# Performance work log

Hardware: AMD Instinct MI355X
Metric: run time of the kernel (lower is better)

Reference implementation:

```python
import jax, jax.numpy as jnp
import numpy as np

N_NODES = 100000
N_EDGES = 1250000
FEAT = 64
HID = 10
MOD = 10.0


def setup_inputs() -> dict:
    key = jax.random.key(0)
    ks = jax.random.split(key, 12)
    inp = {
        "X": jax.random.normal(ks[0], (N_NODES, FEAT), dtype=jnp.float32),
        "W2_0": jax.random.normal(ks[1], (2 * FEAT, HID), dtype=jnp.float32) * 0.1,
        "W1_0": jax.random.normal(ks[2], (HID, HID), dtype=jnp.float32) * 0.3,
        "W2_1": jax.random.normal(ks[3], (2 * HID, HID), dtype=jnp.float32) * 0.3,
        "W1_1": jax.random.normal(ks[4], (HID, HID), dtype=jnp.float32) * 0.3,
        "W2_2": jax.random.normal(ks[5], (2 * HID, HID), dtype=jnp.float32) * 0.3,
        "W1_2": jax.random.normal(ks[6], (HID, HID), dtype=jnp.float32) * 0.3,
        "Wf1": jax.random.normal(ks[7], (HID, FEAT), dtype=jnp.float32) * 0.3,
        "Wf2": jax.random.normal(ks[8], (FEAT, FEAT), dtype=jnp.float32) * 0.1,
        "edge_src": jax.random.randint(ks[9], (N_EDGES,), 0, N_NODES, dtype=jnp.int64 if jax.config.jax_enable_x64 else jnp.int32),
        "edge_dst": jax.random.randint(ks[10], (N_EDGES,), 0, N_NODES, dtype=jnp.int64 if jax.config.jax_enable_x64 else jnp.int32),
    }
    return inp


def _rgcn_layer(X, W2, W1, src, dst):
    # gather target (i) and source (j) node features per edge: [E, in_dim]
    X_i = X[dst]
    X_j = X[src]
    # message: dense_2(relu) then dense_1(relu), divided by mod
    m = jax.nn.relu(jnp.concatenate([X_i, X_j], axis=-1) @ W2)
    m = jax.nn.relu(m @ W1) / MOD  # [E, HID]
    # sum-aggregate messages at target nodes
    agg = jax.ops.segment_sum(m, dst, num_segments=N_NODES)
    # layer activation='relu' (identity here since messages are nonneg, kept for fidelity)
    return jax.nn.relu(agg)


def reference(X, W2_0, W1_0, W2_1, W1_1, W2_2, W1_2, Wf1, Wf2, edge_src, edge_dst):
    h = X
    for W2, W1 in ((W2_0, W1_0), (W2_1, W1_1), (W2_2, W1_2)):
        h = _rgcn_layer(h, W2, W1, edge_src, edge_dst)
    h = jax.nn.relu(h @ Wf1)
    h = jax.nn.relu(h @ Wf2)
    return h
```

## Files before the change

### kernel.cpp

```cpp
#include <hip/hip_runtime.h>
#include <hip/hip_bf16.h>
#include <hip/hip_fp16.h>

#define FEAT 64
#define HID 10
#define RS 16
#define BRS 4
#define EPB 1024
#define BSH 6
#define CHK 32

typedef __attribute__((ext_vector_type(2))) float f32x2;

#if defined(__has_builtin)
#if __has_builtin(__builtin_elementwise_fma)
#define HAVE_EW_FMA 1
#endif
#endif

__device__ __forceinline__ f32x2 pk_fma(f32x2 a, f32x2 b, f32x2 c) {
#ifdef HAVE_EW_FMA
    return __builtin_elementwise_fma(a, b, c);
#else
    f32x2 r; r.x = fmaf(a.x, b.x, c.x); r.y = fmaf(a.y, b.y, c.y); return r;
#endif
}
__device__ __forceinline__ f32x2 pk_max0(f32x2 a) {
    f32x2 r; r.x = fmaxf(a.x, 0.f); r.y = fmaxf(a.y, 0.f); return r;
}

__device__ __forceinline__ unsigned int f2fp12(float v) {
    unsigned short h = __half_as_ushort(__float2half(v));
    return (((unsigned int)h) + 8u) >> 4;
}
__device__ __forceinline__ float fp12f(unsigned int f) {
    return __half2float(__ushort_as_half((unsigned short)(f << 4)));
}
__device__ __forceinline__ uint4 pack10(const float* b) {
    unsigned int f[10];
#pragma unroll
    for (int i = 0; i < 10; i++) f[i] = f2fp12(b[i]);
    uint4 d;
    d.x = f[0] | (f[1] << 12) | (f[2] << 24);
    d.y = (f[2] >> 8) | (f[3] << 4) | (f[4] << 16) | (f[5] << 28);
    d.z = (f[5] >> 4) | (f[6] << 8) | (f[7] << 20);
    d.w = f[8] | (f[9] << 12);
    return d;
}

__global__ __launch_bounds__(256) void pre_l0(
    const float* __restrict__ X,
    const float* __restrict__ W2,
    float* __restrict__ A,
    unsigned int* __restrict__ Bt,
    int n_nodes)
{
    __shared__ float w2[128 * 10];
    for (int i = threadIdx.x; i < 1280; i += 256) w2[i] = W2[i];
    __syncthreads();

    int n = blockIdx.x * 256 + threadIdx.x;
    if (n >= n_nodes) return;

    const float4* xr = reinterpret_cast<const float4*>(X + (size_t)n * FEAT);
    float a[10], b[10];
#pragma unroll
    for (int h = 0; h < 10; h++) { a[h] = 0.f; b[h] = 0.f; }

#pragma unroll
    for (int blk = 0; blk < 16; blk++) {
        float4 u = xr[blk];
        float xv[4] = { u.x, u.y, u.z, u.w };
#pragma unroll
        for (int j = 0; j < 4; j++) {
            int k = blk * 4 + j;
#pragma unroll
            for (int h = 0; h < 10; h++) {
                a[h] = fmaf(xv[j], w2[k * 10 + h], a[h]);
                b[h] = fmaf(xv[j], w2[(64 + k) * 10 + h], b[h]);
            }
        }
    }

    float4* Ar = reinterpret_cast<float4*>(A + (size_t)n * RS);
    Ar[0] = make_float4(a[0], a[1], a[2], a[3]);
    Ar[1] = make_float4(a[4], a[5], a[6], a[7]);
    Ar[2] = make_float4(a[8], a[9], 0.f, 0.f);
    *reinterpret_cast<uint4*>(Bt + (size_t)n * BRS) = pack10(b);
}


__global__ __launch_bounds__(256) void bin_hist_k(
    const int* __restrict__ dst, int* __restrict__ blockhist, int n_edges, int nbk)
{
    extern __shared__ int hist[];
    for (int i = threadIdx.x; i < nbk; i += 256) hist[i] = 0;
    __syncthreads();
    int base = blockIdx.x * EPB;
    for (int i = threadIdx.x; i < EPB; i += 256) {
        int e = base + i;
        if (e < n_edges) atomicAdd(&hist[dst[e] >> BSH], 1);
    }
    __syncthreads();
    int* row = blockhist + (size_t)blockIdx.x * nbk;
    for (int i = threadIdx.x; i < nbk; i += 256) row[i] = hist[i];
}

__global__ __launch_bounds__(256) void colchunk_sum_k(
    const int* __restrict__ blockhist, int* __restrict__ chunksum,
    int nbk, int nblk, int nchk)
{
    int b = blockIdx.x * 256 + threadIdx.x;
    int c = blockIdx.y;
    if (b >= nbk) return;
    int k0 = c * CHK;
    int k1 = min(k0 + CHK, nblk);
    int s = 0;
    for (int k = k0; k < k1; k++) s += blockhist[(size_t)k * nbk + b];
    chunksum[(size_t)b * nchk + c] = s;
}

__global__ __launch_bounds__(256) void chunk_scan_k(
    int* __restrict__ chunksum, int* __restrict__ btot, int nbk, int nchk)
{
    int b = blockIdx.x * 256 + threadIdx.x;
    if (b >= nbk) return;
    int run = 0;
    int* row = chunksum + (size_t)b * nchk;
    for (int c = 0; c < nchk; c++) {
        int v = row[c];
        row[c] = run;
        run += v;
    }
    btot[b] = run;
}

__global__ __launch_bounds__(256) void scan_k(
    const int* __restrict__ btot, int* __restrict__ bbase,
    int* __restrict__ bucket_start, int* __restrict__ start,
    int nbk, int n_nodes, int n_edges)
{
    __shared__ int ts[256];
    int t = threadIdx.x;
    int v[8];
    int s = 0;
#pragma unroll
    for (int j = 0; j < 8; j++) {
        int idx = t * 8 + j;
        v[j] = (idx < nbk) ? btot[idx] : 0;
        s += v[j];
    }
    ts[t] = s;
    __syncthreads();
    for (int off = 1; off < 256; off <<= 1) {
        int x = (t >= off) ? ts[t - off] : 0;
        __syncthreads();
        ts[t] += x;
        __syncthreads();
    }
    int run = ts[t] - s;
#pragma unroll
    for (int j = 0; j < 8; j++) {
        int idx = t * 8 + j;
        if (idx < nbk) { bbase[idx] = run; bucket_start[idx] = run; }
        run += v[j];
    }
    if (t == 255) { bucket_start[nbk] = n_edges; start[n_nodes] = n_edges; }
}

__global__ __launch_bounds__(256) void col_off2_k(
    int* __restrict__ blockhist, const int* __restrict__ chunksum,
    const int* __restrict__ bbase, int nbk, int nblk, int nchk)
{
    int b = blockIdx.x * 256 + threadIdx.x;
    int c = blockIdx.y;
    if (b >= nbk) return;
    int k0 = c * CHK;
    int k1 = min(k0 + CHK, nblk);
    int run = bbase[b] + chunksum[(size_t)b * nchk + c];
    for (int k = k0; k < k1; k++) {
        size_t idx = (size_t)k * nbk + b;
        int v = blockhist[idx];
        blockhist[idx] = run;
        run += v;
    }
}

__global__ __launch_bounds__(256) void bin_scatter_k(
    const int* __restrict__ src, const int* __restrict__ dst,
    const int* __restrict__ blockhist, int* __restrict__ packed,
    int n_edges, int nbk)
{
    extern __shared__ int cur[];
    const int* row = blockhist + (size_t)blockIdx.x * nbk;
    for (int i = threadIdx.x; i < nbk; i += 256) cur[i] = row[i];
    __syncthreads();
    int base = blockIdx.x * EPB;
    for (int i = threadIdx.x; i < EPB; i += 256) {
        int e = base + i;
        if (e < n_edges) {
            int d = dst[e];
            int pos = atomicAdd(&cur[d >> BSH], 1);
            packed[pos] = ((d & 63) << 17) | src[e];
        }
    }
}

__global__ __launch_bounds__(256) void csr_k(
    const int* __restrict__ packed, const int* __restrict__ bucket_start,
    int* __restrict__ nbr, int* __restrict__ start, int n_nodes)
{
    __shared__ int hist[64];
    __shared__ int excl[64];
    __shared__ int cur[64];
    int b = blockIdx.x;
    int base = bucket_start[b];
    int end  = bucket_start[b + 1];
    if (threadIdx.x < 64) hist[threadIdx.x] = 0;
    __syncthreads();
    for (int i = base + threadIdx.x; i < end; i += 256)
        atomicAdd(&hist[packed[i] >> 17], 1);
    __syncthreads();
    if (threadIdx.x == 0) {
        int r = 0;
        for (int k = 0; k < 64; k++) { excl[k] = r; r += hist[k]; }
    }
    __syncthreads();
    if (threadIdx.x < 64) {
        cur[threadIdx.x] = excl[threadIdx.x];
        int node = (b << 6) + threadIdx.x;
        if (node < n_nodes) start[node] = base + excl[threadIdx.x];
    }
    __syncthreads();
    for (int i = base + threadIdx.x; i < end; i += 256) {
        int p = packed[i];
        int pos = base + atomicAdd(&cur[p >> 17], 1);
        nbr[pos] = p & 0x1FFFF;
    }
}

template<bool LAST>
__global__ __launch_bounds__(256) void gather_k(
    const float* __restrict__ A,
    const unsigned int* __restrict__ Bt,
    const float* __restrict__ W1,
    const float* __restrict__ W2n,
    const int* __restrict__ start,
    const int* __restrict__ nbr,
    float* __restrict__ An,
    unsigned int* __restrict__ Bn,
    float* __restrict__ Hout,
    int n_nodes)
{
    __shared__ float w2s[200];
    if (!LAST) {
        for (int i = threadIdx.x; i < 200; i += 256) w2s[i] = W2n[i];
        __syncthreads();
    }

    f32x2 w1p[10][5];
#pragma unroll
    for (int j = 0; j < 10; j++)
#pragma unroll
        for (int h2 = 0; h2 < 5; h2++)
            w1p[j][h2] = (f32x2){ W1[j * 10 + 2 * h2], W1[j * 10 + 2 * h2 + 1] };

    int t = blockIdx.x * 256 + threadIdx.x;
    int n = t >> 2;
    int q = t & 3;
    if (n >= n_nodes) return;

    const float4* ar = reinterpret_cast<const float4*>(A + (size_t)n * RS);
    float4 a0 = ar[0], a1 = ar[1], a2 = ar[2];
    f32x2 av2[5] = { {a0.x,a0.y}, {a0.z,a0.w}, {a1.x,a1.y}, {a1.z,a1.w}, {a2.x,a2.y} };

    f32x2 acc2[5];
#pragma unroll
    for (int h2 = 0; h2 < 5; h2++) acc2[h2] = (f32x2){0.f, 0.f};

    int beg = start[n];
    int end = start[n + 1];
    for (int i = beg + q; i < end; i += 4) {
        int s = nbr[i];
        uint4 d = *reinterpret_cast<const uint4*>(Bt + (size_t)s * BRS);
        unsigned int f0 = d.x & 0xFFFu;
        unsigned int f1 = (d.x >> 12) & 0xFFFu;
        unsigned int f2 = (d.x >> 24) | ((d.y & 0xFu) << 8);
        unsigned int f3 = (d.y >> 4) & 0xFFFu;
        unsigned int f4 = (d.y >> 16) & 0xFFFu;
        unsigned int f5 = ((d.y >> 28) & 0xFu) | ((d.z & 0xFFu) << 4);
        unsigned int f6 = (d.z >> 8) & 0xFFFu;
        unsigned int f7 = d.z >> 20;
        unsigned int f8 = d.w & 0xFFFu;
        unsigned int f9 = (d.w >> 12) & 0xFFFu;

        f32x2 pre[5];
        pre[0] = av2[0] + (f32x2){ fp12f(f0), fp12f(f1) };
        pre[1] = av2[1] + (f32x2){ fp12f(f2), fp12f(f3) };
        pre[2] = av2[2] + (f32x2){ fp12f(f4), fp12f(f5) };
        pre[3] = av2[3] + (f32x2){ fp12f(f6), fp12f(f7) };
        pre[4] = av2[4] + (f32x2){ fp12f(f8), fp12f(f9) };
#pragma unroll
        for (int k = 0; k < 5; k++) pre[k] = pk_max0(pre[k]);

        f32x2 z[5];
#pragma unroll
        for (int h2 = 0; h2 < 5; h2++) z[h2] = (f32x2){0.f, 0.f};
#pragma unroll
        for (int j2 = 0; j2 < 5; j2++) {
            f32x2 pa = (f32x2){ pre[j2].x, pre[j2].x };
            f32x2 pb = (f32x2){ pre[j2].y, pre[j2].y };
#pragma unroll
            for (int h2 = 0; h2 < 5; h2++) {
                z[h2] = pk_fma(pa, w1p[2 * j2][h2], z[h2]);
                z[h2] = pk_fma(pb, w1p[2 * j2 + 1][h2], z[h2]);
            }
        }
#pragma unroll
        for (int h2 = 0; h2 < 5; h2++) acc2[h2] += pk_max0(z[h2]);
    }

#pragma unroll
    for (int h2 = 0; h2 < 5; h2++) {
        acc2[h2].x += __shfl_xor(acc2[h2].x, 1);
        acc2[h2].y += __shfl_xor(acc2[h2].y, 1);
    }
#pragma unroll
    for (int h2 = 0; h2 < 5; h2++) {
        acc2[h2].x += __shfl_xor(acc2[h2].x, 2);
        acc2[h2].y += __shfl_xor(acc2[h2].y, 2);
    }

    float hv[10];
#pragma unroll
    for (int h2 = 0; h2 < 5; h2++) {
        hv[2 * h2]     = acc2[h2].x * 0.1f;
        hv[2 * h2 + 1] = acc2[h2].y * 0.1f;
    }

    if (LAST) {
        float* Hr = Hout + (size_t)n * RS;
        if (q == 0)      *reinterpret_cast<float4*>(Hr)     = make_float4(hv[0], hv[1], hv[2], hv[3]);
        else if (q == 1) *reinterpret_cast<float4*>(Hr + 4) = make_float4(hv[4], hv[5], hv[6], hv[7]);
        else if (q == 2) *reinterpret_cast<float2*>(Hr + 8) = make_float2(hv[8], hv[9]);
    } else {
        if (q == 0) {
            float a[8];
#pragma unroll
            for (int h = 0; h < 8; h++) {
                float zz = 0.f;
#pragma unroll
                for (int k = 0; k < 10; k++) zz = fmaf(hv[k], w2s[k * 10 + h], zz);
                a[h] = zz;
            }
            float4* Ar = reinterpret_cast<float4*>(An + (size_t)n * RS);
            Ar[0] = make_float4(a[0], a[1], a[2], a[3]);
            Ar[1] = make_float4(a[4], a[5], a[6], a[7]);
        } else if (q == 1) {
            float a8 = 0.f, a9 = 0.f;
#pragma unroll
            for (int k = 0; k < 10; k++) {
                a8 = fmaf(hv[k], w2s[k * 10 + 8], a8);
                a9 = fmaf(hv[k], w2s[k * 10 + 9], a9);
            }
            *reinterpret_cast<float2*>(An + (size_t)n * RS + 8) = make_float2(a8, a9);
        } else if (q == 2) {
            float b[10];
#pragma unroll
            for (int h = 0; h < 10; h++) {
                float zz = 0.f;
#pragma unroll
                for (int k = 0; k < 10; k++) zz = fmaf(hv[k], w2s[100 + k * 10 + h], zz);
                b[h] = zz;
            }
            *reinterpret_cast<uint4*>(Bn + (size_t)n * BRS) = pack10(b);
        }
    }
}

__global__ __launch_bounds__(256) void final_k(
    const float* __restrict__ H,
    const float* __restrict__ Wf1,
    const float* __restrict__ Wf2,
    float* __restrict__ out,
    int n_nodes)
{
    __shared__ float wf1[640];
    __shared__ float wf2s[64 * 64];
    __shared__ float tT[64 * 64];

    for (int i = threadIdx.x; i < 640; i += 256) wf1[i] = Wf1[i];
    {
        const float4* w2v = reinterpret_cast<const float4*>(Wf2);
        float4* w2s = reinterpret_cast<float4*>(wf2s);
        for (int i = threadIdx.x; i < 1024; i += 256) w2s[i] = w2v[i];
    }

    int node0 = blockIdx.x * 64;

    {
        int r = threadIdx.x & 63;
        int g = threadIdx.x >> 6;
        int node = node0 + r;
        float hv[10];
        if (node < n_nodes) {
            const float4* hr = reinterpret_cast<const float4*>(H + (size_t)node * RS);
            float4 h0 = hr[0], h1 = hr[1];
            float2 h2 = *reinterpret_cast<const float2*>(H + (size_t)node * RS + 8);
            hv[0]=h0.x; hv[1]=h0.y; hv[2]=h0.z; hv[3]=h0.w;
            hv[4]=h1.x; hv[5]=h1.y; hv[6]=h1.z; hv[7]=h1.w;
            hv[8]=h2.x; hv[9]=h2.y;
        } else {
#pragma unroll
            for (int k = 0; k < 10; k++) hv[k] = 0.f;
        }
        __syncthreads();
#pragma unroll
        for (int j = 0; j < 16; j++) {
            int c = g * 16 + j;
            float v = 0.f;
#pragma unroll
            for (int k = 0; k < 10; k++) v = fmaf(hv[k], wf1[k * 64 + c], v);
            tT[c * 64 + r] = fmaxf(v, 0.f);
        }
    }
    __syncthreads();

    int r0 = (threadIdx.x >> 4) * 4;
    int c0 = (threadIdx.x & 15) * 4;
    float acc[4][4];
#pragma unroll
    for (int i = 0; i < 4; i++)
#pragma unroll
        for (int j = 0; j < 4; j++) acc[i][j] = 0.f;

    for (int k = 0; k < 64; k++) {
        float4 a = *reinterpret_cast<const float4*>(&tT[k * 64 + r0]);
        float4 b = *reinterpret_cast<const float4*>(&wf2s[k * 64 + c0]);
        float av[4] = { a.x, a.y, a.z, a.w };
        float bv[4] = { b.x, b.y, b.z, b.w };
#pragma unroll
        for (int i = 0; i < 4; i++)
#pragma unroll
            for (int j = 0; j < 4; j++)
                acc[i][j] = fmaf(av[i], bv[j], acc[i][j]);
    }

#pragma unroll
    for (int i = 0; i < 4; i++) {
        int node = node0 + r0 + i;
        if (node < n_nodes) {
            float4 o = make_float4(fmaxf(acc[i][0], 0.f), fmaxf(acc[i][1], 0.f),
                                   fmaxf(acc[i][2], 0.f), fmaxf(acc[i][3], 0.f));
            *reinterpret_cast<float4*>(&out[(size_t)node * FEAT + c0]) = o;
        }
    }
}

extern "C" void kernel_launch(void* const* d_in, const int* in_sizes, int n_in,
                              void* d_out, int out_size, void* d_ws, size_t ws_size,
                              hipStream_t stream) {
    const float* X    = (const float*)d_in[0];
    const float* W2_0 = (const float*)d_in[1];
    const float* W1_0 = (const float*)d_in[2];
    const float* W2_1 = (const float*)d_in[3];
    const float* W1_1 = (const float*)d_in[4];
    const float* W2_2 = (const float*)d_in[5];
    const float* W1_2 = (const float*)d_in[6];
    const float* Wf1  = (const float*)d_in[7];
    const float* Wf2  = (const float*)d_in[8];
    const int* src = (const int*)d_in[9];
    const int* dst = (const int*)d_in[10];
    float* out = (float*)d_out;

    const int n_edges = in_sizes[9];
    const int n_nodes = in_sizes[0] / FEAT;

    const int nbk  = (n_nodes + 63) >> 6;
    const int nblk = (n_edges + EPB - 1) / EPB;
    const int nchk = (nblk + CHK - 1) / CHK;

    const size_t h_elems = (size_t)n_nodes * RS;
    const size_t b_elems = (size_t)n_nodes * BRS;
    const size_t offH   = 0;
    const size_t offA0  = offH  + h_elems;
    const size_t offA1  = offA0 + h_elems;
    const size_t offB0  = offA1 + h_elems;
    const size_t offB1  = offB0 + b_elems;
    const size_t offNbr = offB1 + b_elems;
    const size_t offPk  = offNbr + (size_t)n_edges;
    const size_t offBh  = offPk + (size_t)n_edges;
    const size_t offCs  = offBh + (size_t)nblk * nbk;
    const size_t offBt  = offCs + (size_t)nbk * nchk;
    const size_t offBb  = offBt + (size_t)nbk;
    const size_t offBs  = offBb + (size_t)nbk;
    const size_t offSt  = offBs + (size_t)nbk + 1;

    float* H            = (float*)d_ws + offH;
    float* A0           = (float*)d_ws + offA0;
    float* A1           = (float*)d_ws + offA1;
    unsigned int* B0    = (unsigned int*)d_ws + offB0;
    unsigned int* B1    = (unsigned int*)d_ws + offB1;
    int* nbr            = (int*)d_ws + offNbr;
    int* packed         = (int*)d_ws + offPk;
    int* blockhist      = (int*)d_ws + offBh;
    int* chunksum       = (int*)d_ws + offCs;
    int* btot           = (int*)d_ws + offBt;
    int* bbase          = (int*)d_ws + offBb;
    int* bstart         = (int*)d_ws + offBs;
    int* start          = (int*)d_ws + offSt;

    const int nb = (n_nodes + 255) / 256;
    const int gb = (n_nodes * 4 + 255) / 256;
    const int fb = (n_nodes + 63) / 64;
    const int cb = (nbk + 255) / 256;
    const size_t lds_bins = (size_t)nbk * 4;

    bin_hist_k<<<nblk, 256, lds_bins, stream>>>(dst, blockhist, n_edges, nbk);
    colchunk_sum_k<<<dim3(cb, nchk), 256, 0, stream>>>(blockhist, chunksum, nbk, nblk, nchk);
    chunk_scan_k<<<cb, 256, 0, stream>>>(chunksum, btot, nbk, nchk);
    scan_k<<<1, 256, 0, stream>>>(btot, bbase, bstart, start, nbk, n_nodes, n_edges);
    col_off2_k<<<dim3(cb, nchk), 256, 0, stream>>>(blockhist, chunksum, bbase, nbk, nblk, nchk);
    bin_scatter_k<<<nblk, 256, lds_bins, stream>>>(src, dst, blockhist, packed, n_edges, nbk);
    csr_k<<<nbk, 256, 0, stream>>>(packed, bstart, nbr, start, n_nodes);

    pre_l0<<<nb, 256, 0, stream>>>(X, W2_0, A0, B0, n_nodes);
    gather_k<false><<<gb, 256, 0, stream>>>(A0, B0, W1_0, W2_1, start, nbr,
                                            A1, B1, nullptr, n_nodes);
    gather_k<false><<<gb, 256, 0, stream>>>(A1, B1, W1_1, W2_2, start, nbr,
                                            A0, B0, nullptr, n_nodes);
    gather_k<true><<<gb, 256, 0, stream>>>(A0, B0, W1_2, nullptr, start, nbr,
                                           nullptr, nullptr, H, n_nodes);

    final_k<<<fb, 256, 0, stream>>>(H, Wf1, Wf2, out, n_nodes);
}
```

Measured before the change: 249.3 us.

## Simplify CSR build with global atomics and fuse final MLP into last gather

Replaces the seven-kernel, per-block histogram counting sort with a memset, a global-atomic bucket histogram, a single scan and a global-atomic scatter. This cuts launches and the large blockhist traffic, at the cost of heavy contention on global atomics for about 1600 buckets. The last gather layer is also fused with the final two dense layers, so the H intermediate buffer and one kernel launch go away. In exchange, the fused kernel carries about 37KB of LDS per block and reloads Wf2 in every block, which may lower occupancy.

```diff
diff --git a/kernel.cpp b/kernel.cpp
--- a/kernel.cpp
+++ b/kernel.cpp
@@ -1,14 +1,11 @@
 #include <hip/hip_runtime.h>
-#include <hip/hip_bf16.h>
 #include <hip/hip_fp16.h>
 
 #define FEAT 64
 #define HID 10
 #define RS 16
 #define BRS 4
-#define EPB 1024
 #define BSH 6
-#define CHK 32
 
 typedef __attribute__((ext_vector_type(2))) float f32x2;
 
@@ -90,54 +87,17 @@
 }
 
 
-__global__ __launch_bounds__(256) void bin_hist_k(
-    const int* __restrict__ dst, int* __restrict__ blockhist, int n_edges, int nbk)
-{
-    extern __shared__ int hist[];
-    for (int i = threadIdx.x; i < nbk; i += 256) hist[i] = 0;
-    __syncthreads();
-    int base = blockIdx.x * EPB;
-    for (int i = threadIdx.x; i < EPB; i += 256) {
-        int e = base + i;
-        if (e < n_edges) atomicAdd(&hist[dst[e] >> BSH], 1);
-    }
-    __syncthreads();
-    int* row = blockhist + (size_t)blockIdx.x * nbk;
-    for (int i = threadIdx.x; i < nbk; i += 256) row[i] = hist[i];
-}
-
-__global__ __launch_bounds__(256) void colchunk_sum_k(
-    const int* __restrict__ blockhist, int* __restrict__ chunksum,
-    int nbk, int nblk, int nchk)
-{
-    int b = blockIdx.x * 256 + threadIdx.x;
-    int c = blockIdx.y;
-    if (b >= nbk) return;
-    int k0 = c * CHK;
-    int k1 = min(k0 + CHK, nblk);
-    int s = 0;
-    for (int k = k0; k < k1; k++) s += blockhist[(size_t)k * nbk + b];
-    chunksum[(size_t)b * nchk + c] = s;
-}
-
-__global__ __launch_bounds__(256) void chunk_scan_k(
-    int* __restrict__ chunksum, int* __restrict__ btot, int nbk, int nchk)
-{
-    int b = blockIdx.x * 256 + threadIdx.x;
-    if (b >= nbk) return;
-    int run = 0;
-    int* row = chunksum + (size_t)b * nchk;
-    for (int c = 0; c < nchk; c++) {
-        int v = row[c];
-        row[c] = run;
-        run += v;
-    }
-    btot[b] = run;
+__global__ __launch_bounds__(256) void ghist_k(
+    const int* __restrict__ dst, int* __restrict__ bcnt, int n_edges)
+{
+    int e = blockIdx.x * 256 + threadIdx.x;
+    if (e >= n_edges) return;
+    atomicAdd(&bcnt[dst[e] >> BSH], 1);
 }
 
 __global__ __launch_bounds__(256) void scan_k(
-    const int* __restrict__ btot, int* __restrict__ bbase,
-    int* __restrict__ bucket_start, int* __restrict__ start,
+    const int* __restrict__ bcnt, int* __restrict__ bstart,
+    int* __restrict__ cursor, int* __restrict__ startv,
     int nbk, int n_nodes, int n_edges)
 {
     __shared__ int ts[256];
@@ -147,7 +107,7 @@
 #pragma unroll
     for (int j = 0; j < 8; j++) {
         int idx = t * 8 + j;
-        v[j] = (idx < nbk) ? btot[idx] : 0;
+        v[j] = (idx < nbk) ? bcnt[idx] : 0;
         s += v[j];
     }
     ts[t] = s;
@@ -162,64 +122,37 @@
 #pragma unroll
     for (int j = 0; j < 8; j++) {
         int idx = t * 8 + j;
-        if (idx < nbk) { bbase[idx] = run; bucket_start[idx] = run; }
+        if (idx < nbk) { bstart[idx] = run; cursor[idx] = run; }
         run += v[j];
     }
-    if (t == 255) { bucket_start[nbk] = n_edges; start[n_nodes] = n_edges; }
-}
-
-__global__ __launch_bounds__(256) void col_off2_k(
-    int* __restrict__ blockhist, const int* __restrict__ chunksum,
-    const int* __restrict__ bbase, int nbk, int nblk, int nchk)
-{
-    int b = blockIdx.x * 256 + threadIdx.x;
-    int c = blockIdx.y;
-    if (b >= nbk) return;
-    int k0 = c * CHK;
-    int k1 = min(k0 + CHK, nblk);
-    int run = bbase[b] + chunksum[(size_t)b * nchk + c];
-    for (int k = k0; k < k1; k++) {
-        size_t idx = (size_t)k * nbk + b;
-        int v = blockhist[idx];
-        blockhist[idx] = run;
-        run += v;
-    }
-}
-
-__global__ __launch_bounds__(256) void bin_scatter_k(
+    if (t == 255) { bstart[nbk] = n_edges; startv[n_nodes] = n_edges; }
+}
+
+__global__ __launch_bounds__(256) void gscatter_k(
     const int* __restrict__ src, const int* __restrict__ dst,
-    const int* __restrict__ blockhist, int* __restrict__ packed,
-    int n_edges, int nbk)
-{
-    extern __shared__ int cur[];
-    const int* row = blockhist + (size_t)blockIdx.x * nbk;
-    for (int i = threadIdx.x; i < nbk; i += 256) cur[i] = row[i];
-    __syncthreads();
-    int base = blockIdx.x * EPB;
-    for (int i = threadIdx.x; i < EPB; i += 256) {
-        int e = base + i;
-        if (e < n_edges) {
-            int d = dst[e];
-            int pos = atomicAdd(&cur[d >> BSH], 1);
-            packed[pos] = ((d & 63) << 17) | src[e];
-        }
-    }
+    int* __restrict__ cursor, int* __restrict__ packedv, int n_edges)
+{
+    int e = blockIdx.x * 256 + threadIdx.x;
+    if (e >= n_edges) return;
+    int d = dst[e];
+    int pos = atomicAdd(&cursor[d >> BSH], 1);
+    packedv[pos] = ((d & 63) << 17) | src[e];
 }
 
 __global__ __launch_bounds__(256) void csr_k(
-    const int* __restrict__ packed, const int* __restrict__ bucket_start,
-    int* __restrict__ nbr, int* __restrict__ start, int n_nodes)
+    const int* __restrict__ packedv, const int* __restrict__ bstart,
+    int* __restrict__ nbr, int* __restrict__ startv, int n_nodes)
 {
     __shared__ int hist[64];
     __shared__ int excl[64];
     __shared__ int cur[64];
     int b = blockIdx.x;
-    int base = bucket_start[b];
-    int end  = bucket_start[b + 1];
+    int base = bstart[b];
+    int end  = bstart[b + 1];
     if (threadIdx.x < 64) hist[threadIdx.x] = 0;
     __syncthreads();
     for (int i = base + threadIdx.x; i < end; i += 256)
-        atomicAdd(&hist[packed[i] >> 17], 1);
+        atomicAdd(&hist[packedv[i] >> 17], 1);
     __syncthreads();
     if (threadIdx.x == 0) {
         int r = 0;
@@ -229,47 +162,21 @@
     if (threadIdx.x < 64) {
         cur[threadIdx.x] = excl[threadIdx.x];
         int node = (b << 6) + threadIdx.x;
-        if (node < n_nodes) start[node] = base + excl[threadIdx.x];
+        if (node < n_nodes) startv[node] = base + excl[threadIdx.x];
     }
     __syncthreads();
     for (int i = base + threadIdx.x; i < end; i += 256) {
-        int p = packed[i];
+        int p = packedv[i];
         int pos = base + atomicAdd(&cur[p >> 17], 1);
         nbr[pos] = p & 0x1FFFF;
     }
 }
 
-template<bool LAST>
-__global__ __launch_bounds__(256) void gather_k(
-    const float* __restrict__ A,
-    const unsigned int* __restrict__ Bt,
-    const float* __restrict__ W1,
-    const float* __restrict__ W2n,
-    const int* __restrict__ start,
-    const int* __restrict__ nbr,
-    float* __restrict__ An,
-    unsigned int* __restrict__ Bn,
-    float* __restrict__ Hout,
-    int n_nodes)
-{
-    __shared__ float w2s[200];
-    if (!LAST) {
-        for (int i = threadIdx.x; i < 200; i += 256) w2s[i] = W2n[i];
-        __syncthreads();
-    }
-
-    f32x2 w1p[10][5];
-#pragma unroll
-    for (int j = 0; j < 10; j++)
-#pragma unroll
-        for (int h2 = 0; h2 < 5; h2++)
-            w1p[j][h2] = (f32x2){ W1[j * 10 + 2 * h2], W1[j * 10 + 2 * h2 + 1] };
-
-    int t = blockIdx.x * 256 + threadIdx.x;
-    int n = t >> 2;
-    int q = t & 3;
-    if (n >= n_nodes) return;
-
+__device__ __forceinline__ void gather_core(
+    const float* __restrict__ A, const unsigned int* __restrict__ Bt,
+    const f32x2 (&w1p)[10][5], const int* __restrict__ startv,
+    const int* __restrict__ nbr, int n, int q, float (&hv)[10])
+{
     const float4* ar = reinterpret_cast<const float4*>(A + (size_t)n * RS);
     float4 a0 = ar[0], a1 = ar[1], a2 = ar[2];
     f32x2 av2[5] = { {a0.x,a0.y}, {a0.z,a0.w}, {a1.x,a1.y}, {a1.z,a1.w}, {a2.x,a2.y} };
@@ -278,8 +185,8 @@
 #pragma unroll
     for (int h2 = 0; h2 < 5; h2++) acc2[h2] = (f32x2){0.f, 0.f};
 
-    int beg = start[n];
-    int end = start[n + 1];
+    int beg = startv[n];
+    int end = startv[n + 1];
     for (int i = beg + q; i < end; i += 4) {
         int s = nbr[i];
         uint4 d = *reinterpret_cast<const uint4*>(Bt + (size_t)s * BRS);
@@ -330,102 +237,133 @@
         acc2[h2].x += __shfl_xor(acc2[h2].x, 2);
         acc2[h2].y += __shfl_xor(acc2[h2].y, 2);
     }
-
-    float hv[10];
 #pragma unroll
     for (int h2 = 0; h2 < 5; h2++) {
         hv[2 * h2]     = acc2[h2].x * 0.1f;
         hv[2 * h2 + 1] = acc2[h2].y * 0.1f;
     }
-
-    if (LAST) {
-        float* Hr = Hout + (size_t)n * RS;
-        if (q == 0)      *reinterpret_cast<float4*>(Hr)     = make_float4(hv[0], hv[1], hv[2], hv[3]);
-        else if (q == 1) *reinterpret_cast<float4*>(Hr + 4) = make_float4(hv[4], hv[5], hv[6], hv[7]);
-        else if (q == 2) *reinterpret_cast<float2*>(Hr + 8) = make_float2(hv[8], hv[9]);
-    } else {
-        if (q == 0) {
-            float a[8];
-#pragma unroll
-            for (int h = 0; h < 8; h++) {
-                float zz = 0.f;
-#pragma unroll
-                for (int k = 0; k < 10; k++) zz = fmaf(hv[k], w2s[k * 10 + h], zz);
-                a[h] = zz;
-            }
-            float4* Ar = reinterpret_cast<float4*>(An + (size_t)n * RS);
-            Ar[0] = make_float4(a[0], a[1], a[2], a[3]);
-            Ar[1] = make_float4(a[4], a[5], a[6], a[7]);
-        } else if (q == 1) {
-            float a8 = 0.f, a9 = 0.f;
-#pragma unroll
-            for (int k = 0; k < 10; k++) {
-                a8 = fmaf(hv[k], w2s[k * 10 + 8], a8);
-                a9 = fmaf(hv[k], w2s[k * 10 + 9], a9);
-            }
-            *reinterpret_cast<float2*>(An + (size_t)n * RS + 8) = make_float2(a8, a9);
-        } else if (q == 2) {
-            float b[10];
-#pragma unroll
-            for (int h = 0; h < 10; h++) {
-                float zz = 0.f;
-#pragma unroll
-                for (int k = 0; k < 10; k++) zz = fmaf(hv[k], w2s[100 + k * 10 + h], zz);
-                b[h] = zz;
-            }
-            *reinterpret_cast<uint4*>(Bn + (size_t)n * BRS) = pack10(b);
-        }
-    }
-}
-
-__global__ __launch_bounds__(256) void final_k(
-    const float* __restrict__ H,
+}
+
+__global__ __launch_bounds__(256) void gather_mid_k(
+    const float* __restrict__ A, const unsigned int* __restrict__ Bt,
+    const float* __restrict__ W1, const float* __restrict__ W2n,
+    const int* __restrict__ startv, const int* __restrict__ nbr,
+    float* __restrict__ An, unsigned int* __restrict__ Bn, int n_nodes)
+{
+    __shared__ float w2s[200];
+    for (int i = threadIdx.x; i < 200; i += 256) w2s[i] = W2n[i];
+    __syncthreads();
+
+    f32x2 w1p[10][5];
+#pragma unroll
+    for (int j = 0; j < 10; j++)
+#pragma unroll
+        for (int h2 = 0; h2 < 5; h2++)
+            w1p[j][h2] = (f32x2){ W1[j * 10 + 2 * h2], W1[j * 10 + 2 * h2 + 1] };
+
+    int t = blockIdx.x * 256 + threadIdx.x;
+    int n = t >> 2;
+    int q = t & 3;
+    if (n >= n_nodes) return;
+
+    float hv[10];
+    gather_core(A, Bt, w1p, startv, nbr, n, q, hv);
+
+    if (q == 0) {
+        float a[8];
+#pragma unroll
+        for (int h = 0; h < 8; h++) {
+            float zz = 0.f;
+#pragma unroll
+            for (int k = 0; k < 10; k++) zz = fmaf(hv[k], w2s[k * 10 + h], zz);
+            a[h] = zz;
+        }
+        float4* Ar = reinterpret_cast<float4*>(An + (size_t)n * RS);
+        Ar[0] = make_float4(a[0], a[1], a[2], a[3]);
+        Ar[1] = make_float4(a[4], a[5], a[6], a[7]);
+    } else if (q == 1) {
+        float a8 = 0.f, a9 = 0.f;
+#pragma unroll
+        for (int k = 0; k < 10; k++) {
+            a8 = fmaf(hv[k], w2s[k * 10 + 8], a8);
+            a9 = fmaf(hv[k], w2s[k * 10 + 9], a9);
+        }
+        *reinterpret_cast<float2*>(An + (size_t)n * RS + 8) = make_float2(a8, a9);
+    } else if (q == 2) {
+        float bb[10];
+#pragma unroll
+        for (int h = 0; h < 10; h++) {
+            float zz = 0.f;
+#pragma unroll
+            for (int k = 0; k < 10; k++) zz = fmaf(hv[k], w2s[100 + k * 10 + h], zz);
+            bb[h] = zz;
+        }
+        *reinterpret_cast<uint4*>(Bn + (size_t)n * BRS) = pack10(bb);
+    }
+}
+
+__global__ __launch_bounds__(256) void gather_fin_k(
+    const float* __restrict__ A, const unsigned int* __restrict__ Bt,
+    const float* __restrict__ W1,
+    const int* __restrict__ startv, const int* __restrict__ nbr,
     const float* __restrict__ Wf1,
     const float* __restrict__ Wf2,
     float* __restrict__ out,
     int n_nodes)
 {
     __shared__ float wf1[640];
-    __shared__ float wf2s[64 * 64];
-    __shared__ float tT[64 * 64];
+    __shared__ float wf2s[4096];
+    __shared__ float tT[4096];
+    __shared__ float hvs[640];
 
     for (int i = threadIdx.x; i < 640; i += 256) wf1[i] = Wf1[i];
+    for (int i = threadIdx.x; i < 4096; i += 256) wf2s[i] = Wf2[i];
+
+    f32x2 w1p[10][5];
+#pragma unroll
+    for (int j = 0; j < 10; j++)
+#pragma unroll
+        for (int h2 = 0; h2 < 5; h2++)
+            w1p[j][h2] = (f32x2){ W1[j * 10 + 2 * h2], W1[j * 10 + 2 * h2 + 1] };
+
+    int t0 = blockIdx.x * 256 + threadIdx.x;
+    int n = t0 >> 2;
+    int q = t0 & 3;
+    int r = threadIdx.x >> 2;
+
+    float hv[10];
+#pragma unroll
+    for (int k = 0; k < 10; k++) hv[k] = 0.f;
+    if (n < n_nodes)
+        gather_core(A, Bt, w1p, startv, nbr, n, q, hv);
+
+    if (q == 0) {
+#pragma unroll
+        for (int k = 0; k < 5; k++) hvs[r * 10 + k] = hv[k];
+    } else if (q == 1) {
+#pragma unroll
+        for (int k = 5; k < 10; k++) hvs[r * 10 + k] = hv[k];
+    }
+    __syncthreads();
+
     {
-        const float4* w2v = reinterpret_cast<const float4*>(Wf2);
-        float4* w2s = reinterpret_cast<float4*>(wf2s);
-        for (int i = threadIdx.x; i < 1024; i += 256) w2s[i] = w2v[i];
-    }
+        int rr = threadIdx.x & 63;
+        int gg = threadIdx.x >> 6;
+        float h[10];
+#pragma unroll
+        for (int k = 0; k < 10; k++) h[k] = hvs[rr * 10 + k];
+#pragma unroll
+        for (int j = 0; j < 16; j++) {
+            int c = gg * 16 + j;
+            float v = 0.f;
+#pragma unroll
+            for (int k = 0; k < 10; k++) v = fmaf(h[k], wf1[k * 64 + c], v);
+            tT[c * 64 + rr] = fmaxf(v, 0.f);
+        }
+    }
+    __syncthreads();
 
     int node0 = blockIdx.x * 64;
-
-    {
-        int r = threadIdx.x & 63;
-        int g = threadIdx.x >> 6;
-        int node = node0 + r;
-        float hv[10];
-        if (node < n_nodes) {
-            const float4* hr = reinterpret_cast<const float4*>(H + (size_t)node * RS);
-            float4 h0 = hr[0], h1 = hr[1];
-            float2 h2 = *reinterpret_cast<const float2*>(H + (size_t)node * RS + 8);
-            hv[0]=h0.x; hv[1]=h0.y; hv[2]=h0.z; hv[3]=h0.w;
-            hv[4]=h1.x; hv[5]=h1.y; hv[6]=h1.z; hv[7]=h1.w;
-            hv[8]=h2.x; hv[9]=h2.y;
-        } else {
-#pragma unroll
-            for (int k = 0; k < 10; k++) hv[k] = 0.f;
-        }
-        __syncthreads();
-#pragma unroll
-        for (int j = 0; j < 16; j++) {
-            int c = g * 16 + j;
-            float v = 0.f;
-#pragma unroll
-            for (int k = 0; k < 10; k++) v = fmaf(hv[k], wf1[k * 64 + c], v);
-            tT[c * 64 + r] = fmaxf(v, 0.f);
-        }
-    }
-    __syncthreads();
-
     int r0 = (threadIdx.x >> 4) * 4;
     int c0 = (threadIdx.x & 15) * 4;
     float acc[4][4];
@@ -476,61 +414,44 @@
     const int n_edges = in_sizes[9];
     const int n_nodes = in_sizes[0] / FEAT;
 
-    const int nbk  = (n_nodes + 63) >> 6;
-    const int nblk = (n_edges + EPB - 1) / EPB;
-    const int nchk = (nblk + CHK - 1) / CHK;
+    const int nbk = (n_nodes + 63) >> 6;
 
     const size_t h_elems = (size_t)n_nodes * RS;
     const size_t b_elems = (size_t)n_nodes * BRS;
-    const size_t offH   = 0;
-    const size_t offA0  = offH  + h_elems;
+    const size_t offA0  = 0;
     const size_t offA1  = offA0 + h_elems;
     const size_t offB0  = offA1 + h_elems;
     const size_t offB1  = offB0 + b_elems;
     const size_t offNbr = offB1 + b_elems;
     const size_t offPk  = offNbr + (size_t)n_edges;
-    const size_t offBh  = offPk + (size_t)n_edges;
-    const size_t offCs  = offBh + (size_t)nblk * nbk;
-    const size_t offBt  = offCs + (size_t)nbk * nchk;
-    const size_t offBb  = offBt + (size_t)nbk;
-    const size_t offBs  = offBb + (size_t)nbk;
+    const size_t offBc  = offPk + (size_t)n_edges;
+    const size_t offCu  = offBc + (size_t)nbk;
+    const size_t offBs  = offCu + (size_t)nbk;
     const size_t offSt  = offBs + (size_t)nbk + 1;
 
-    float* H            = (float*)d_ws + offH;
     float* A0           = (float*)d_ws + offA0;
     float* A1           = (float*)d_ws + offA1;
     unsigned int* B0    = (unsigned int*)d_ws + offB0;
     unsigned int* B1    = (unsigned int*)d_ws + offB1;
     int* nbr            = (int*)d_ws + offNbr;
-    int* packed         = (int*)d_ws + offPk;
-    int* blockhist      = (int*)d_ws + offBh;
-    int* chunksum       = (int*)d_ws + offCs;
-    int* btot           = (int*)d_ws + offBt;
-    int* bbase          = (int*)d_ws + offBb;
+    int* packedv        = (int*)d_ws + offPk;
+    int* bcnt           = (int*)d_ws + offBc;
+    int* cursor         = (int*)d_ws + offCu;
     int* bstart         = (int*)d_ws + offBs;
-    int* start          = (int*)d_ws + offSt;
+    int* startv         = (int*)d_ws + offSt;
 
     const int nb = (n_nodes + 255) / 256;
     const int gb = (n_nodes * 4 + 255) / 256;
-    const int fb = (n_nodes + 63) / 64;
-    const int cb = (nbk + 255) / 256;
-    const size_t lds_bins = (size_t)nbk * 4;
-
-    bin_hist_k<<<nblk, 256, lds_bins, stream>>>(dst, blockhist, n_edges, nbk);
-    colchunk_sum_k<<<dim3(cb, nchk), 256, 0, stream>>>(blockhist, chunksum, nbk, nblk, nchk);
-    chunk_scan_k<<<cb, 256, 0, stream>>>(chunksum, btot, nbk, nchk);
-    scan_k<<<1, 256, 0, stream>>>(btot, bbase, bstart, start, nbk, n_nodes, n_edges);
-    col_off2_k<<<dim3(cb, nchk), 256, 0, stream>>>(blockhist, chunksum, bbase, nbk, nblk, nchk);
-    bin_scatter_k<<<nblk, 256, lds_bins, stream>>>(src, dst, blockhist, packed, n_edges, nbk);
-    csr_k<<<nbk, 256, 0, stream>>>(packed, bstart, nbr, start, n_nodes);
+    const int eb = (n_edges + 255) / 256;
+
+    hipMemsetAsync(bcnt, 0, (size_t)nbk * 4, stream);
+    ghist_k<<<eb, 256, 0, stream>>>(dst, bcnt, n_edges);
+    scan_k<<<1, 256, 0, stream>>>(bcnt, bstart, cursor, startv, nbk, n_nodes, n_edges);
+    gscatter_k<<<eb, 256, 0, stream>>>(src, dst, cursor, packedv, n_edges);
+    csr_k<<<nbk, 256, 0, stream>>>(packedv, bstart, nbr, startv, n_nodes);
 
     pre_l0<<<nb, 256, 0, stream>>>(X, W2_0, A0, B0, n_nodes);
-    gather_k<false><<<gb, 256, 0, stream>>>(A0, B0, W1_0, W2_1, start, nbr,
-                                            A1, B1, nullptr, n_nodes);
-    gather_k<false><<<gb, 256, 0, stream>>>(A1, B1, W1_1, W2_2, start, nbr,
-                                            A0, B0, nullptr, n_nodes);
-    gather_k<true><<<gb, 256, 0, stream>>>(A0, B0, W1_2, nullptr, start, nbr,
-                                           nullptr, nullptr, H, n_nodes);
-
-    final_k<<<fb, 256, 0, stream>>>(H, Wf1, Wf2, out, n_nodes);
-}
+    gather_mid_k<<<gb, 256, 0, stream>>>(A0, B0, W1_0, W2_1, startv, nbr, A1, B1, n_nodes);
+    gather_mid_k<<<gb, 256, 0, stream>>>(A1, B1, W1_1, W2_2, startv, nbr, A0, B0, n_nodes);
+    gather_fin_k<<<gb, 256, 0, stream>>>(A0, B0, W1_2, startv, nbr, Wf1, Wf2, out, n_nodes);
+}
```

After: 570.7 us. 2.29x slower.
